# Kernel tuning notes

Measured on AMD Instinct MI355X. Metric: run time of the kernel, lower is better.

## Reference

```python
import jax, jax.numpy as jnp
import numpy as np

N, D, E = 16384, 256, 8
H = D // 2  # gate hidden


def setup_inputs() -> dict:
    key = jax.random.key(0)
    ks = jax.random.split(key, 10)
    s = lambda fan_in: 1.0 / np.sqrt(fan_in)
    return {
        "x":   jax.random.normal(ks[0], (N, D), dtype=jnp.float32),
        # gate: Linear(D, D//2) -> ReLU -> Linear(D//2, E) -> Softmax
        "Wg1": jax.random.uniform(ks[1], (D, H), jnp.float32, -s(D), s(D)),
        "bg1": jax.random.uniform(ks[2], (H,), jnp.float32, -s(D), s(D)),
        "Wg2": jax.random.uniform(ks[3], (H, E), jnp.float32, -s(H), s(H)),
        "bg2": jax.random.uniform(ks[4], (E,), jnp.float32, -s(H), s(H)),
        # experts: per-expert Linear(D,D) -> ReLU -> (Dropout eval=identity) -> Linear(D,D)
        "W1": jax.random.uniform(ks[5], (E, D, D), jnp.float32, -s(D), s(D)),
        "b1": jax.random.uniform(ks[6], (E, D), jnp.float32, -s(D), s(D)),
        "W2": jax.random.uniform(ks[7], (E, D, D), jnp.float32, -s(D), s(D)),
        "b2": jax.random.uniform(ks[8], (E, D), jnp.float32, -s(D), s(D)),
    }


def reference(x, Wg1, bg1, Wg2, bg2, W1, b1, W2, b2):
    # gate: [N, E] softmax over experts
    g = jax.nn.softmax(jax.nn.relu(x @ Wg1 + bg1) @ Wg2 + bg2, axis=-1)
    # all experts applied densely via batched GEMMs (fuses the Python loop)
    h = jax.nn.relu(jnp.einsum("nd,edh->neh", x, W1) + b1)  # [N, E, D]
    y = jnp.einsum("neh,ehd->ned", h, W2) + b2              # [N, E, D]
    # weighted combine: sum_e g[n,e] * y[n,e,:]
    return jnp.einsum("ned,ne->nd", y, g)
```

## Files before the change

### kernel.cpp

```cpp
#include <hip/hip_runtime.h>


typedef unsigned short USH;
typedef float f32x4 __attribute__((ext_vector_type(4)));
typedef __bf16 bf16x8 __attribute__((ext_vector_type(8)));

__device__ __forceinline__ USH f2bf(float f) {
  unsigned int u = __float_as_uint(f);
  u += 0x7fffu + ((u >> 16) & 1u);
  return (USH)(u >> 16);
}


__global__ __launch_bounds__(256) void k_prep(
    const float* __restrict__ Wg1,
    const float* __restrict__ W1,
    const float* __restrict__ W2,
    USH* __restrict__ w1f, USH* __restrict__ w2f, USH* __restrict__ wg1f) {
  __shared__ float T[64][65];
  int b = blockIdx.x, tid = threadIdx.x;

  if (b < 128) {
    int e = b >> 4, tl = b & 15;
    int c0 = (tl >> 2) * 64, h0 = (tl & 3) * 64;
    const float* src = W1 + (size_t)e * 65536;
#pragma unroll
    for (int p = 0; p < 4; ++p) {
      int r = p * 16 + (tid >> 4), d4 = (tid & 15) * 4;
      float4 v = *(const float4*)(src + (size_t)(c0 + r) * 256 + h0 + d4);
      T[r][d4] = v.x; T[r][d4 + 1] = v.y; T[r][d4 + 2] = v.z; T[r][d4 + 3] = v.w;
    }
    __syncthreads();
#pragma unroll
    for (int p = 0; p < 4; ++p) {
      int hr = p * 16 + (tid >> 4), c4 = (tid & 15) * 4;
      USH w[4];
#pragma unroll
      for (int j = 0; j < 4; ++j) w[j] = f2bf(T[c4 + j][hr]);
      int h = h0 + hr;
      int t = h >> 4, lh = h & 15;
      int kt = c0 >> 6, ch = (c4 >> 5) & 1, q = (c4 >> 3) & 3, u0 = c4 & 7;
      size_t idx = ((size_t)((e * 64 + kt * 16 + t) * 2 + ch)) * 512 + (q * 16 + lh) * 8 + u0;
      *(uint2*)(w1f + idx) = *(const uint2*)w;
    }
  } else if (b < 256) {
    int bp = b - 128;
    int e = bp >> 4, tl = bp & 15;
    int h0 = (tl >> 2) * 64, d0 = (tl & 3) * 64;
    const float* src = W2 + (size_t)e * 65536;
#pragma unroll
    for (int p = 0; p < 4; ++p) {
      int r = p * 16 + (tid >> 4), d4 = (tid & 15) * 4;
      float4 v = *(const float4*)(src + (size_t)(h0 + r) * 256 + d0 + d4);
      T[r][d4] = v.x; T[r][d4 + 1] = v.y; T[r][d4 + 2] = v.z; T[r][d4 + 3] = v.w;
    }
    __syncthreads();
#pragma unroll
    for (int p = 0; p < 4; ++p) {
      int dr = p * 16 + (tid >> 4), h4 = (tid & 15) * 4;
      USH w[4];
#pragma unroll
      for (int j = 0; j < 4; ++j) w[j] = f2bf(T[h4 + j][dr]);
      int d = d0 + dr;
      int t = d >> 4, ld = d & 15;
      int ht = h0 >> 6, ch = (h4 >> 5) & 1, q = (h4 >> 3) & 3, u0 = h4 & 7;
      size_t idx = ((size_t)((e * 64 + ht * 16 + t) * 2 + ch)) * 512 + (q * 16 + ld) * 8 + u0;
      *(uint2*)(w2f + idx) = *(const uint2*)w;
    }
  } else {
    int bp = b - 256;
    int c0 = (bp >> 1) * 64, h0 = (bp & 1) * 64;
#pragma unroll
    for (int p = 0; p < 4; ++p) {
      int r = p * 16 + (tid >> 4), d4 = (tid & 15) * 4;
      float4 v = *(const float4*)(Wg1 + (size_t)(c0 + r) * 128 + h0 + d4);
      T[r][d4] = v.x; T[r][d4 + 1] = v.y; T[r][d4 + 2] = v.z; T[r][d4 + 3] = v.w;
    }
    __syncthreads();
#pragma unroll
    for (int p = 0; p < 4; ++p) {
      int hr = p * 16 + (tid >> 4), c4 = (tid & 15) * 4;
      USH w[4];
#pragma unroll
      for (int j = 0; j < 4; ++j) w[j] = f2bf(T[c4 + j][hr]);
      int h = h0 + hr;
      int t = h >> 4, lh = h & 15;
      int kt = c0 >> 6, ch = (c4 >> 5) & 1, q = (c4 >> 3) & 3, u0 = c4 & 7;
      size_t idx = ((size_t)((kt * 8 + t) * 2 + ch)) * 512 + (q * 16 + lh) * 8 + u0;
      *(uint2*)(wg1f + idx) = *(const uint2*)w;
    }
  }
}


__global__ __launch_bounds__(512) void k_moe(const float* __restrict__ x,
                                             const USH* __restrict__ w1f,
                                             const USH* __restrict__ w2f,
                                             const USH* __restrict__ wg1f,
                                             const float* __restrict__ wg2,
                                             const float* __restrict__ bg1,
                                             const float* __restrict__ bg2,
                                             const float* __restrict__ b1,
                                             const float* __restrict__ b2,
                                             float* __restrict__ out) {
  __shared__ __align__(16) USH xs[4 * 64 * 64];
  __shared__ __align__(16) USH Hs[2][64 * 256];
  __shared__ float b1s[2048];
  __shared__ float b2s[2048];
  __shared__ float gse[512];
  __shared__ float wg2t[8 * 132];
  __shared__ float lgg[512];
  __shared__ float bg1s[128];
  __shared__ float bg2g[8];

  int tid = threadIdx.x;
  int wave = tid >> 6, lane = tid & 63;
  int quad = lane >> 4, l16 = lane & 15;
  int sw = l16 & 7;
  int rowBase = blockIdx.x * 64;
  float* hgs = (float*)&Hs[0][0];

#pragma unroll
  for (int it = 0; it < 4; ++it) {
    int i = it * 512 + tid;
    int kt = i >> 9, rem = i & 511;
    int r = rem >> 3, slot = rem & 7;
    int c8 = slot ^ (r & 7);
    const float* sp = x + (size_t)(rowBase + r) * 256 + kt * 64 + c8 * 8;
    float4 a = *(const float4*)sp;
    float4 bq = *(const float4*)(sp + 4);
    USH v[8];
    v[0] = f2bf(a.x);  v[1] = f2bf(a.y);  v[2] = f2bf(a.z);  v[3] = f2bf(a.w);
    v[4] = f2bf(bq.x); v[5] = f2bf(bq.y); v[6] = f2bf(bq.z); v[7] = f2bf(bq.w);
    *(uint4*)(xs + (size_t)i * 8) = *(const uint4*)v;
  }
#pragma unroll
  for (int t = 0; t < 4; ++t) {
    b1s[t * 512 + tid] = b1[t * 512 + tid];
    b2s[t * 512 + tid] = b2[t * 512 + tid];
  }
  for (int t = tid; t < 1024; t += 512) wg2t[(t & 7) * 132 + (t >> 3)] = wg2[t];
  if (tid < 128) bg1s[tid] = bg1[tid];
  if (tid < 8) bg2g[tid] = bg2[tid];

  bf16x8 wra[8], wrb[8];
  auto LDWH = [&](bf16x8* dst, const USH* We, int tb) {
#pragma unroll
    for (int k = 0; k < 2; ++k)
#pragma unroll
      for (int c = 0; c < 2; ++c)
#pragma unroll
        for (int i = 0; i < 2; ++i)
          dst[k * 4 + c * 2 + i] = *(const bf16x8*)(
              We + (size_t)(((tb + k) * 16 + wave * 2 + i) * 2 + c) * 512 + lane * 8);
  };
  LDWH(wra, w1f, 0);
  LDWH(wrb, w1f, 2);

  asm volatile("s_waitcnt lgkmcnt(0)" ::: "memory");
  __builtin_amdgcn_s_barrier();

  {
    f32x4 hg4[4] = {};
#pragma unroll
    for (int kt = 0; kt < 4; ++kt)
#pragma unroll
      for (int c = 0; c < 2; ++c) {
        int cs = ((c * 4 + quad) ^ sw) * 8;
        bf16x8 av = *(const bf16x8*)(wg1f + (size_t)((kt * 8 + wave) * 2 + c) * 512 + lane * 8);
        bf16x8 bv[4];
#pragma unroll
        for (int j = 0; j < 4; ++j)
          bv[j] = *(const bf16x8*)(xs + kt * 4096 + (j * 16 + l16) * 64 + cs);
#pragma unroll
        for (int j = 0; j < 4; ++j)
          hg4[j] = __builtin_amdgcn_mfma_f32_16x16x32_bf16(av, bv[j], hg4[j], 0, 0, 0);
      }
    int hb = wave * 16 + quad * 4;
    int slotbase = wave * 4 + quad;
#pragma unroll
    for (int j = 0; j < 4; ++j) {
      int n = j * 16 + l16;
      int slot = slotbase ^ (n & 7);
      f32x4 v;
#pragma unroll
      for (int r = 0; r < 4; ++r) v[r] = fmaxf(hg4[j][r] + bg1s[hb + r], 0.0f);
      *(f32x4*)(hgs + n * 128 + slot * 4) = v;
    }
  }
  asm volatile("s_waitcnt lgkmcnt(0)" ::: "memory");
  __builtin_amdgcn_s_barrier();

  {
    int n = tid >> 3, eg = tid & 7;
    float s = bg2g[eg];
#pragma unroll
    for (int k4 = 0; k4 < 32; ++k4) {
      int slot = k4 ^ (n & 7);
      f32x4 hv = *(const f32x4*)(hgs + n * 128 + slot * 4);
      const float* wv = wg2t + eg * 132 + k4 * 4;
      s += hv[0] * wv[0]; s += hv[1] * wv[1]; s += hv[2] * wv[2]; s += hv[3] * wv[3];
    }
    lgg[tid] = s;
  }
  asm volatile("s_waitcnt lgkmcnt(0)" ::: "memory");
  __builtin_amdgcn_s_barrier();

  if (tid < 64) {
    float l[8]; float m = -1e30f;
#pragma unroll
    for (int e = 0; e < 8; ++e) { l[e] = lgg[tid * 8 + e]; m = fmaxf(m, l[e]); }
    float s = 0.0f;
#pragma unroll
    for (int e = 0; e < 8; ++e) { l[e] = expf(l[e] - m); s += l[e]; }
    float inv = 1.0f / s;
#pragma unroll
    for (int e = 0; e < 8; ++e) gse[e * 64 + tid] = l[e] * inv;
  }
  asm volatile("s_waitcnt lgkmcnt(0)" ::: "memory");
  __builtin_amdgcn_s_barrier();

  f32x4 oacc[4][2] = {};

#pragma unroll 1
  for (int e = 0; e < 8; ++e) {
    const USH* W2e = w2f + (size_t)e * 65536;
    const USH* W1n = w1f + (size_t)((e + 1) & 7) * 65536;
    f32x4 hacc[2][4] = {};

#pragma unroll
    for (int kt = 0; kt < 2; ++kt)
#pragma unroll
      for (int c = 0; c < 2; ++c) {
        int cs = ((c * 4 + quad) ^ sw) * 8;
        bf16x8 bv[4];
#pragma unroll
        for (int j = 0; j < 4; ++j)
          bv[j] = *(const bf16x8*)(xs + kt * 4096 + (j * 16 + l16) * 64 + cs);
#pragma unroll
        for (int i = 0; i < 2; ++i)
#pragma unroll
          for (int j = 0; j < 4; ++j)
            hacc[i][j] = __builtin_amdgcn_mfma_f32_16x16x32_bf16(
                wra[kt * 4 + c * 2 + i], bv[j], hacc[i][j], 0, 0, 0);
      }
    LDWH(wra, W2e, 0);
#pragma unroll
    for (int kt = 2; kt < 4; ++kt)
#pragma unroll
      for (int c = 0; c < 2; ++c) {
        int cs = ((c * 4 + quad) ^ sw) * 8;
        bf16x8 bv[4];
#pragma unroll
        for (int j = 0; j < 4; ++j)
          bv[j] = *(const bf16x8*)(xs + kt * 4096 + (j * 16 + l16) * 64 + cs);
#pragma unroll
        for (int i = 0; i < 2; ++i)
#pragma unroll
          for (int j = 0; j < 4; ++j)
            hacc[i][j] = __builtin_amdgcn_mfma_f32_16x16x32_bf16(
                wrb[(kt - 2) * 4 + c * 2 + i], bv[j], hacc[i][j], 0, 0, 0);
      }
    LDWH(wrb, W2e, 2);

    USH* Hb = &Hs[e & 1][0];
#pragma unroll
    for (int i = 0; i < 2; ++i) {
      int slot = (wave & 1) * 4 + i * 2 + (quad >> 1);
      int hb = wave * 32 + i * 16 + quad * 4;
#pragma unroll
      for (int j = 0; j < 4; ++j) {
        int n = j * 16 + l16;
        float gg = gse[e * 64 + n];
        USH w4[4];
#pragma unroll
        for (int r = 0; r < 4; ++r)
          w4[r] = f2bf(fmaxf(hacc[i][j][r] + b1s[e * 256 + hb + r], 0.0f) * gg);
        int off = n * 256 + (wave >> 1) * 64 + ((slot ^ (n & 7)) * 8) + (quad & 1) * 4;
        *(uint2*)(Hb + off) = *(const uint2*)w4;
      }
    }

    asm volatile("s_waitcnt lgkmcnt(0)" ::: "memory");
    __builtin_amdgcn_s_barrier();

#pragma unroll
    for (int ht = 0; ht < 2; ++ht)
#pragma unroll
      for (int c = 0; c < 2; ++c) {
        int cs = ((c * 4 + quad) ^ sw) * 8;
        bf16x8 av[4];
#pragma unroll
        for (int i = 0; i < 4; ++i)
          av[i] = *(const bf16x8*)(Hb + (i * 16 + l16) * 256 + ht * 64 + cs);
#pragma unroll
        for (int i = 0; i < 4; ++i)
#pragma unroll
          for (int j = 0; j < 2; ++j)
            oacc[i][j] = __builtin_amdgcn_mfma_f32_16x16x32_bf16(
                av[i], wra[ht * 4 + c * 2 + j], oacc[i][j], 0, 0, 0);
      }
    LDWH(wra, W1n, 0);
#pragma unroll
    for (int ht = 2; ht < 4; ++ht)
#pragma unroll
      for (int c = 0; c < 2; ++c) {
        int cs = ((c * 4 + quad) ^ sw) * 8;
        bf16x8 av[4];
#pragma unroll
        for (int i = 0; i < 4; ++i)
          av[i] = *(const bf16x8*)(Hb + (i * 16 + l16) * 256 + ht * 64 + cs);
#pragma unroll
        for (int i = 0; i < 4; ++i)
#pragma unroll
          for (int j = 0; j < 2; ++j)
            oacc[i][j] = __builtin_amdgcn_mfma_f32_16x16x32_bf16(
                av[i], wrb[(ht - 2) * 4 + c * 2 + j], oacc[i][j], 0, 0, 0);
      }
    LDWH(wrb, W1n, 2);
  }

#pragma unroll
  for (int i = 0; i < 4; ++i)
#pragma unroll
    for (int r = 0; r < 4; ++r) {
      int n = i * 16 + quad * 4 + r;
      size_t grow = (size_t)(rowBase + n) * 256;
#pragma unroll
      for (int j = 0; j < 2; ++j) {
        int d = wave * 32 + j * 16 + l16;
        float bias = 0.0f;
#pragma unroll
        for (int ee = 0; ee < 8; ++ee) bias += gse[ee * 64 + n] * b2s[ee * 256 + d];
        out[grow + d] = oacc[i][j][r] + bias;
      }
    }
}


extern "C" void kernel_launch(void* const* d_in, const int* in_sizes, int n_in,
                              void* d_out, int out_size, void* d_ws, size_t ws_size,
                              hipStream_t stream) {
  const float* x   = (const float*)d_in[0];
  const float* Wg1 = (const float*)d_in[1];
  const float* bg1 = (const float*)d_in[2];
  const float* Wg2 = (const float*)d_in[3];
  const float* bg2 = (const float*)d_in[4];
  const float* W1  = (const float*)d_in[5];
  const float* b1  = (const float*)d_in[6];
  const float* W2  = (const float*)d_in[7];
  const float* b2  = (const float*)d_in[8];
  float* out = (float*)d_out;

  char* ws = (char*)d_ws;
  USH* w1f  = (USH*)(ws + 8388608);
  USH* wg1f = (USH*)(ws + 9437184);
  USH* w2f  = (USH*)(ws + 9502720);

  hipLaunchKernelGGL(k_prep, dim3(264), dim3(256), 0, stream,
                     Wg1, W1, W2, w1f, w2f, wg1f);
  hipLaunchKernelGGL(k_moe, dim3(256), dim3(512), 0, stream,
                     x, w1f, w2f, wg1f, Wg2, bg1, bg2, b1, b2, out);
}
```

Measured before the change: 123.2 us.

## Split experts across two blocks per row tile and combine with atomics

```diff
diff --git a/kernel.cpp b/kernel.cpp
--- a/kernel.cpp
+++ b/kernel.cpp
@@ -93,32 +93,35 @@
 }
 
 
-__global__ __launch_bounds__(512) void k_moe(const float* __restrict__ x,
-                                             const USH* __restrict__ w1f,
-                                             const USH* __restrict__ w2f,
-                                             const USH* __restrict__ wg1f,
-                                             const float* __restrict__ wg2,
-                                             const float* __restrict__ bg1,
-                                             const float* __restrict__ bg2,
-                                             const float* __restrict__ b1,
-                                             const float* __restrict__ b2,
-                                             float* __restrict__ out) {
+__global__ __launch_bounds__(512, 2) void k_moe(
+    const float* __restrict__ x,
+    const USH* __restrict__ w1f,
+    const USH* __restrict__ w2f,
+    const USH* __restrict__ wg1f,
+    const float* __restrict__ wg2,
+    const float* __restrict__ bg1,
+    const float* __restrict__ bg2,
+    const float* __restrict__ b1,
+    const float* __restrict__ b2,
+    float* __restrict__ out) {
   __shared__ __align__(16) USH xs[4 * 64 * 64];
-  __shared__ __align__(16) USH Hs[2][64 * 256];
-  __shared__ float b1s[2048];
-  __shared__ float b2s[2048];
+  __shared__ __align__(16) USH HsB[64 * 256];
+  __shared__ float scr[1192];
+  __shared__ float b2sU[2048];
   __shared__ float gse[512];
-  __shared__ float wg2t[8 * 132];
-  __shared__ float lgg[512];
-  __shared__ float bg1s[128];
-  __shared__ float bg2g[8];
 
   int tid = threadIdx.x;
   int wave = tid >> 6, lane = tid & 63;
   int quad = lane >> 4, l16 = lane & 15;
   int sw = l16 & 7;
-  int rowBase = blockIdx.x * 64;
-  float* hgs = (float*)&Hs[0][0];
+  int g = blockIdx.x >> 1, s = blockIdx.x & 1;
+  int rowBase = g * 64;
+  int eBase = s * 4;
+  float* hgs = (float*)&HsB[0];
+  float* wg2t = scr;
+  float* bg1s = scr + 1056;
+  float* bg2g = scr + 1184;
+  float* lgg = b2sU;
 
 #pragma unroll
   for (int it = 0; it < 4; ++it) {
@@ -134,11 +137,6 @@
     v[4] = f2bf(bq.x); v[5] = f2bf(bq.y); v[6] = f2bf(bq.z); v[7] = f2bf(bq.w);
     *(uint4*)(xs + (size_t)i * 8) = *(const uint4*)v;
   }
-#pragma unroll
-  for (int t = 0; t < 4; ++t) {
-    b1s[t * 512 + tid] = b1[t * 512 + tid];
-    b2s[t * 512 + tid] = b2[t * 512 + tid];
-  }
   for (int t = tid; t < 1024; t += 512) wg2t[(t & 7) * 132 + (t >> 3)] = wg2[t];
   if (tid < 128) bg1s[tid] = bg1[tid];
   if (tid < 8) bg2g[tid] = bg2[tid];
@@ -154,8 +152,9 @@
           dst[k * 4 + c * 2 + i] = *(const bf16x8*)(
               We + (size_t)(((tb + k) * 16 + wave * 2 + i) * 2 + c) * 512 + lane * 8);
   };
-  LDWH(wra, w1f, 0);
-  LDWH(wrb, w1f, 2);
+  const USH* W1base = w1f + (size_t)eBase * 65536;
+  LDWH(wra, W1base, 0);
+  LDWH(wrb, W1base, 2);
 
   asm volatile("s_waitcnt lgkmcnt(0)" ::: "memory");
   __builtin_amdgcn_s_barrier();
@@ -193,15 +192,16 @@
 
   {
     int n = tid >> 3, eg = tid & 7;
-    float s = bg2g[eg];
+    float ssum = bg2g[eg];
 #pragma unroll
     for (int k4 = 0; k4 < 32; ++k4) {
       int slot = k4 ^ (n & 7);
       f32x4 hv = *(const f32x4*)(hgs + n * 128 + slot * 4);
       const float* wv = wg2t + eg * 132 + k4 * 4;
-      s += hv[0] * wv[0]; s += hv[1] * wv[1]; s += hv[2] * wv[2]; s += hv[3] * wv[3];
-    }
-    lgg[tid] = s;
+      ssum += hv[0] * wv[0]; ssum += hv[1] * wv[1];
+      ssum += hv[2] * wv[2]; ssum += hv[3] * wv[3];
+    }
+    lgg[tid] = ssum;
   }
   asm volatile("s_waitcnt lgkmcnt(0)" ::: "memory");
   __builtin_amdgcn_s_barrier();
@@ -210,22 +210,34 @@
     float l[8]; float m = -1e30f;
 #pragma unroll
     for (int e = 0; e < 8; ++e) { l[e] = lgg[tid * 8 + e]; m = fmaxf(m, l[e]); }
-    float s = 0.0f;
-#pragma unroll
-    for (int e = 0; e < 8; ++e) { l[e] = expf(l[e] - m); s += l[e]; }
-    float inv = 1.0f / s;
+    float ssum = 0.0f;
+#pragma unroll
+    for (int e = 0; e < 8; ++e) { l[e] = expf(l[e] - m); ssum += l[e]; }
+    float inv = 1.0f / ssum;
 #pragma unroll
     for (int e = 0; e < 8; ++e) gse[e * 64 + tid] = l[e] * inv;
   }
   asm volatile("s_waitcnt lgkmcnt(0)" ::: "memory");
   __builtin_amdgcn_s_barrier();
 
+  {
+    float* b1s = scr;
+    b1s[tid] = b1[eBase * 256 + tid];
+    b1s[tid + 512] = b1[eBase * 256 + tid + 512];
+#pragma unroll
+    for (int t = 0; t < 4; ++t) b2sU[t * 512 + tid] = b2[t * 512 + tid];
+  }
+  asm volatile("s_waitcnt lgkmcnt(0)" ::: "memory");
+  __builtin_amdgcn_s_barrier();
+
+  float* b1s = scr;
   f32x4 oacc[4][2] = {};
 
 #pragma unroll 1
-  for (int e = 0; e < 8; ++e) {
+  for (int le = 0; le < 4; ++le) {
+    int e = eBase + le;
     const USH* W2e = w2f + (size_t)e * 65536;
-    const USH* W1n = w1f + (size_t)((e + 1) & 7) * 65536;
+    const USH* W1n = w1f + (size_t)(eBase + ((le + 1) & 3)) * 65536;
     f32x4 hacc[2][4] = {};
 
 #pragma unroll
@@ -263,7 +275,6 @@
       }
     LDWH(wrb, W2e, 2);
 
-    USH* Hb = &Hs[e & 1][0];
 #pragma unroll
     for (int i = 0; i < 2; ++i) {
       int slot = (wave & 1) * 4 + i * 2 + (quad >> 1);
@@ -275,9 +286,9 @@
         USH w4[4];
 #pragma unroll
         for (int r = 0; r < 4; ++r)
-          w4[r] = f2bf(fmaxf(hacc[i][j][r] + b1s[e * 256 + hb + r], 0.0f) * gg);
+          w4[r] = f2bf(fmaxf(hacc[i][j][r] + b1s[le * 256 + hb + r], 0.0f) * gg);
         int off = n * 256 + (wave >> 1) * 64 + ((slot ^ (n & 7)) * 8) + (quad & 1) * 4;
-        *(uint2*)(Hb + off) = *(const uint2*)w4;
+        *(uint2*)(HsB + off) = *(const uint2*)w4;
       }
     }
 
@@ -292,7 +303,7 @@
         bf16x8 av[4];
 #pragma unroll
         for (int i = 0; i < 4; ++i)
-          av[i] = *(const bf16x8*)(Hb + (i * 16 + l16) * 256 + ht * 64 + cs);
+          av[i] = *(const bf16x8*)(HsB + (i * 16 + l16) * 256 + ht * 64 + cs);
 #pragma unroll
         for (int i = 0; i < 4; ++i)
 #pragma unroll
@@ -309,7 +320,7 @@
         bf16x8 av[4];
 #pragma unroll
         for (int i = 0; i < 4; ++i)
-          av[i] = *(const bf16x8*)(Hb + (i * 16 + l16) * 256 + ht * 64 + cs);
+          av[i] = *(const bf16x8*)(HsB + (i * 16 + l16) * 256 + ht * 64 + cs);
 #pragma unroll
         for (int i = 0; i < 4; ++i)
 #pragma unroll
@@ -318,6 +329,9 @@
                 av[i], wrb[(ht - 2) * 4 + c * 2 + j], oacc[i][j], 0, 0, 0);
       }
     LDWH(wrb, W1n, 2);
+
+    asm volatile("s_waitcnt lgkmcnt(0)" ::: "memory");
+    __builtin_amdgcn_s_barrier();
   }
 
 #pragma unroll
@@ -329,10 +343,14 @@
 #pragma unroll
       for (int j = 0; j < 2; ++j) {
         int d = wave * 32 + j * 16 + l16;
-        float bias = 0.0f;
-#pragma unroll
-        for (int ee = 0; ee < 8; ++ee) bias += gse[ee * 64 + n] * b2s[ee * 256 + d];
-        out[grow + d] = oacc[i][j][r] + bias;
+        float v = oacc[i][j][r];
+        if (s == 0) {
+          float bias = 0.0f;
+#pragma unroll
+          for (int ee = 0; ee < 8; ++ee) bias += gse[ee * 64 + n] * b2sU[ee * 256 + d];
+          v += bias;
+        }
+        unsafeAtomicAdd(&out[grow + d], v);
       }
     }
 }
@@ -359,6 +377,7 @@
 
   hipLaunchKernelGGL(k_prep, dim3(264), dim3(256), 0, stream,
                      Wg1, W1, W2, w1f, w2f, wg1f);
-  hipLaunchKernelGGL(k_moe, dim3(256), dim3(512), 0, stream,
+  hipMemsetAsync(d_out, 0, (size_t)out_size, stream);
+  hipLaunchKernelGGL(k_moe, dim3(512), dim3(512), 0, stream,
                      x, w1f, w2f, wg1f, Wg2, bg1, bg2, b1, b2, out);
 }
```

After: 154.3 us. 25.3% more time.
